# Performance work log

Hardware: AMD Instinct MI355X
Metric: run time of the kernel (lower is better)

Reference implementation:

```python
import jax, jax.numpy as jnp
import numpy as np

NR_EMB = 4096
D = 128
DECAY = 0.99
EPS = 1e-05
COMMITMENT_WEIGHT = 1.0


def setup_inputs() -> dict:
    key = jax.random.key(0)
    k1, k2 = jax.random.split(key)
    inpt = jax.random.normal(k1, (32, 2048, D), dtype=jnp.float32)
    emb_mtrx = jax.random.normal(k2, (D, NR_EMB), dtype=jnp.float32) * 0.05
    ema_cluster_size = jnp.zeros((NR_EMB,), dtype=jnp.float32)
    ema_dw = emb_mtrx  # build() initializes ema_dw to a copy of emb_mtrx
    return {"inpt": inpt, "emb_mtrx": emb_mtrx,
            "ema_cluster_size": ema_cluster_size, "ema_dw": ema_dw}


def reference(inpt, emb_mtrx, ema_cluster_size, ema_dw):
    # training=True forward: quantize + EMA codebook update
    K = emb_mtrx.shape[1]
    x = inpt.reshape(-1, inpt.shape[-1])  # [N, D]
    dist = (jnp.sum(x * x, axis=1, keepdims=True)
            - 2.0 * (x @ emb_mtrx)
            + jnp.sum(emb_mtrx * emb_mtrx, axis=0, keepdims=True))  # [N, K]
    idx = jnp.argmax(-dist, axis=1)                       # [N]
    idx_oh = jax.nn.one_hot(idx, K, dtype=x.dtype)        # [N, K]

    # EMA updates (moving_average_update: s = s*decay + v*(1-decay))
    new_cluster = ema_cluster_size * DECAY + jnp.sum(idx_oh, axis=0) * (1.0 - DECAY)
    new_dw = ema_dw * DECAY + (x.T @ idx_oh) * (1.0 - DECAY)  # [D, K]
    n = jnp.sum(new_cluster)
    new_emb = new_dw / (n * (new_cluster + 1e-05) / (n + K * 1e-05))[None, :]

    # lookup uses the just-updated codebook (assign happens before lookup in TF eager)
    idx_r = idx.reshape(inpt.shape[:-1])
    q = new_emb.T[idx_r]                                  # [B, T, D]

    l_commitment = jnp.mean((jax.lax.stop_gradient(q) - inpt) ** 2)
    loss = COMMITMENT_WEIGHT * l_commitment
    q = inpt + jax.lax.stop_gradient(q - inpt)            # straight-through

    avg_probs = jnp.mean(idx_oh, axis=0)
    perplexity = jnp.exp(-jnp.sum(avg_probs * jnp.log(avg_probs + 1e-10)))
    return q, loss, perplexity, new_emb, new_cluster, new_dw
```

## Files before the change

### kernel.cpp

```cpp
#include <hip/hip_runtime.h>
#include <cstdint>
#include <cstddef>

#define NR_EMB 4096
#define DD 128
#define NTOT 65536
#define MARGIN 3e-4f
#define RB 16

typedef __attribute__((ext_vector_type(8))) short short8;
typedef __attribute__((ext_vector_type(4))) float f32x4;

#define WS_CNT    0u
#define WS_SCAL   16384u
#define WS_AMBC   16448u
#define WS_COLN   16512u
#define WS_IDX    32896u
#define WS_EMBT   295040u
#define WS_LPART  2392192u
#define WS_ETH    2424960u
#define WS_ETL    3473536u
#define WS_AMBL   4522112u
#define WS_OFF    4784256u
#define WS_CUR    4800640u
#define WS_BKT    4817024u
#define WS_DWT    5079168u

#define OUT_Q      0u
#define OUT_LOSS   8388608u
#define OUT_PERP   8388609u
#define OUT_EMB    8388610u
#define OUT_CLUS   8912898u
#define OUT_DW     8916994u

__device__ __forceinline__ unsigned short f2bf(float f) {
    unsigned u = __float_as_uint(f);
    return (unsigned short)((u + 0x7FFFu + ((u >> 16) & 1u)) >> 16);
}
__device__ __forceinline__ float bf2f(unsigned short h) {
    return __uint_as_float(((unsigned)h) << 16);
}

__global__ __launch_bounds__(128) void k_prep_e(const float* __restrict__ E,
                                                unsigned short* __restrict__ EtHb,
                                                unsigned short* __restrict__ EtLb,
                                                float* __restrict__ coln,
                                                unsigned int* __restrict__ counts,
                                                int* __restrict__ ambC) {
    __shared__ float Es[128][33];
    const int tid = threadIdx.x;
    const int k0  = blockIdx.x * 32;
    if (tid < 32) counts[k0 + tid] = 0u;
    if (blockIdx.x == 0 && tid < 16) ambC[tid] = 0;
    #pragma unroll
    for (int i = 0; i < 32; ++i) {
        int e = i * 128 + tid;
        int d = e >> 5, kc = e & 31;
        Es[d][kc] = E[(size_t)d * NR_EMB + k0 + kc];
    }
    __syncthreads();
    const int kc = tid >> 2, q = tid & 3;
    const int k = k0 + kc;
    const int sw = (k & 7) << 3;
    float cs = 0.f;
    #pragma unroll
    for (int i = 0; i < 32; ++i) {
        float v = Es[q * 32 + i][kc];
        cs = fmaf(v, v, cs);
    }
    #pragma unroll
    for (int j = 0; j < 4; ++j) {
        short8 hv, lv;
        #pragma unroll
        for (int e = 0; e < 8; ++e) {
            int od = q * 32 + j * 8 + e;
            float v = Es[od ^ sw][kc];
            unsigned short h = f2bf(v);
            hv[e] = (short)h;
            lv[e] = (short)f2bf(v - bf2f(h));
        }
        *(short8*)&EtHb[(size_t)k * DD + q * 32 + j * 8] = hv;
        *(short8*)&EtLb[(size_t)k * DD + q * 32 + j * 8] = lv;
    }
    cs += __shfl_xor(cs, 1);
    cs += __shfl_xor(cs, 2);
    if (q == 0) coln[k] = cs;
}

__device__ __forceinline__ void mrg(float& b1, int& i1, float& b2,
                                    float ob1, int oi1, float ob2) {
    bool take = (ob1 < b1) || (ob1 == b1 && oi1 < i1);
    float loser = take ? b1 : ob1;
    b2 = fminf(fminf(b2, ob2), loser);
    if (take) { b1 = ob1; i1 = oi1; }
}

__global__ __launch_bounds__(256, 2) void k_dist(const float* __restrict__ x,
                                                 const unsigned short* __restrict__ EtHb,
                                                 const unsigned short* __restrict__ EtLb,
                                                 const float* __restrict__ coln,
                                                 int* __restrict__ idx_out,
                                                 unsigned int* __restrict__ counts,
                                                 int* __restrict__ ambCnt,
                                                 int* __restrict__ ambList) {
    __shared__ char lds[65536];

    const int tid  = threadIdx.x;
    const int lane = tid & 63;
    const int w    = tid >> 6;
    const int n0   = blockIdx.x * 128;
    const int rowbase = (w >> 1) * 32;
    const int shalf   = (w & 1) * 64;

    auto stage = [&](int kt, int b) {
        const char* gH = (const char*)EtHb + (size_t)kt * 16384;
        const char* gL = (const char*)EtLb + (size_t)kt * 16384;
        char* lH = lds + b * 32768;
        char* lL = lH + 16384;
        int off = tid * 16;
        #pragma unroll
        for (int j = 0; j < 4; ++j) {
            __builtin_amdgcn_global_load_lds(
                (const __attribute__((address_space(1))) unsigned int*)(gH + off + j * 4096),
                (__attribute__((address_space(3))) unsigned int*)(lH + off + j * 4096), 16, 0, 0);
            __builtin_amdgcn_global_load_lds(
                (const __attribute__((address_space(1))) unsigned int*)(gL + off + j * 4096),
                (__attribute__((address_space(3))) unsigned int*)(lL + off + j * 4096), 16, 0, 0);
        }
    };

    stage(0, 0);

    short8 ah[4][4], al[4][4];
    #pragma unroll
    for (int m = 0; m < 4; ++m) {
        int samp = n0 + shalf + m * 16 + (lane & 15);
        const float* xp = x + (size_t)samp * DD + ((lane >> 4) * 8);
        #pragma unroll
        for (int t = 0; t < 4; ++t) {
            float4 f0 = *(const float4*)(xp + t * 32);
            float4 f1 = *(const float4*)(xp + t * 32 + 4);
            float fv[8] = {f0.x, f0.y, f0.z, f0.w, f1.x, f1.y, f1.z, f1.w};
            short8 h, l;
            #pragma unroll
            for (int j = 0; j < 8; ++j) {
                unsigned short hh = f2bf(fv[j]);
                h[j] = (short)hh;
                l[j] = (short)f2bf(fv[j] - bf2f(hh));
            }
            ah[m][t] = h;
            al[m][t] = l;
        }
    }
    __syncthreads();

    float b1[4][4], b2[4][4];
    int   kb[4][4];
    #pragma unroll
    for (int m = 0; m < 4; ++m)
        #pragma unroll
        for (int r = 0; r < 4; ++r) { b1[m][r] = 3.4e38f; b2[m][r] = 3.4e38f; kb[m][r] = 0; }

    int buf = 0;
    for (int kt = 0; kt < 64; ++kt) {
        if (kt < 63) stage(kt + 1, buf ^ 1);
        const char* lH = lds + buf * 32768;
        const char* lL = lH + 16384;

        #pragma unroll
        for (int n = 0; n < 2; ++n) {
            int row = rowbase + n * 16 + (lane & 15);
            size_t rbo = (size_t)row << 8;
            unsigned swz = (unsigned)((row & 7) << 4);
            float cn = coln[kt * 64 + row];
            int enc = kt * 2 + n;

            f32x4 acc[4];
            #pragma unroll
            for (int m = 0; m < 4; ++m) acc[m] = (f32x4){0.f, 0.f, 0.f, 0.f};

            __builtin_amdgcn_s_setprio(1);
            #pragma unroll
            for (int t = 0; t < 4; ++t) {
                unsigned coff = ((unsigned)(t * 64 + ((lane >> 4) << 4))) ^ swz;
                short8 bh = *(const short8*)(lH + rbo + coff);
                short8 bl = *(const short8*)(lL + rbo + coff);
                #pragma unroll
                for (int m = 0; m < 4; ++m)
                    acc[m] = __builtin_amdgcn_mfma_f32_16x16x32_bf16(ah[m][t], bh, acc[m], 0, 0, 0);
                #pragma unroll
                for (int m = 0; m < 4; ++m)
                    acc[m] = __builtin_amdgcn_mfma_f32_16x16x32_bf16(al[m][t], bh, acc[m], 0, 0, 0);
                #pragma unroll
                for (int m = 0; m < 4; ++m)
                    acc[m] = __builtin_amdgcn_mfma_f32_16x16x32_bf16(ah[m][t], bl, acc[m], 0, 0, 0);
            }
            __builtin_amdgcn_s_setprio(0);

            #pragma unroll
            for (int m = 0; m < 4; ++m) {
                #pragma unroll
                for (int r = 0; r < 4; ++r) {
                    float d = fmaf(-2.f, acc[m][r], cn);
                    bool lt = d < b1[m][r];
                    b2[m][r] = __builtin_amdgcn_fmed3f(d, b1[m][r], b2[m][r]);
                    b1[m][r] = fminf(b1[m][r], d);
                    kb[m][r] = lt ? enc : kb[m][r];
                }
            }
        }
        __syncthreads();
        buf ^= 1;
    }

    float* sb1 = (float*)lds;
    int*   si1 = (int*)(lds + 1024);
    float* sb2 = (float*)(lds + 2048);

    #pragma unroll
    for (int m = 0; m < 4; ++m) {
        #pragma unroll
        for (int r = 0; r < 4; ++r) {
            float B1 = b1[m][r];
            int   I1 = (kb[m][r] >> 1) * 64 + rowbase + (kb[m][r] & 1) * 16 + (lane & 15);
            float B2 = b2[m][r];
            #pragma unroll
            for (int msk = 1; msk < 16; msk <<= 1) {
                float ob1 = __shfl_xor(B1, msk);
                int   oi1 = __shfl_xor(I1, msk);
                float ob2 = __shfl_xor(B2, msk);
                mrg(B1, I1, B2, ob1, oi1, ob2);
            }
            if ((lane & 15) == 0) {
                int sl = shalf + m * 16 + ((lane >> 4) << 2) + r;
                int ch = w >> 1;
                sb1[ch * 128 + sl] = B1;
                si1[ch * 128 + sl] = I1;
                sb2[ch * 128 + sl] = B2;
            }
        }
    }
    __syncthreads();
    if (tid < 128) {
        float B1 = sb1[tid]; int I1 = si1[tid]; float B2 = sb2[tid];
        mrg(B1, I1, B2, sb1[128 + tid], si1[128 + tid], sb2[128 + tid]);
        idx_out[n0 + tid] = I1;
        atomicAdd(&counts[I1], 1u);
        if (B2 - B1 < MARGIN) {
            int p = atomicAdd(ambCnt, 1);
            ambList[p] = n0 + tid;
        }
    }
}

__global__ __launch_bounds__(256) void k_rescore(const float* __restrict__ x,
                                                 const float* __restrict__ E,
                                                 const float* __restrict__ coln,
                                                 const int* __restrict__ ambCnt,
                                                 const int* __restrict__ ambList,
                                                 float* __restrict__ pval,
                                                 int* __restrict__ pidx) {
    __shared__ float xs[RB][DD];
    __shared__ float xn[RB];
    __shared__ float rb1[RB][256];
    __shared__ int   ri1[RB][256];

    const int tid = threadIdx.x;
    const int cnt = *ambCnt;
    const int nbatch = (cnt + RB - 1) / RB;
    const int nwork = nbatch * 8;

    for (int wk = blockIdx.x; wk < nwork; wk += gridDim.x) {
        const int b  = wk >> 3;
        const int ch = wk & 7;
        const int e0 = b * RB;
        const int nb = min(RB, cnt - e0);
        __syncthreads();
        #pragma unroll
        for (int p = 0; p < 2; ++p) {
            int slot = p * 256 + tid;
            int e = slot >> 5, c = slot & 31;
            if (e < nb) {
                int s = ambList[e0 + e];
                *(float4*)&xs[e][c * 4] = *(const float4*)&x[(size_t)s * DD + c * 4];
            } else {
                float4 z; z.x = z.y = z.z = z.w = 0.f;
                *(float4*)&xs[e][c * 4] = z;
            }
        }
        __syncthreads();
        if (tid < RB) {
            float a = 0.f;
            for (int d = 0; d < DD; ++d) a = fmaf(xs[tid][d], xs[tid][d], a);
            xn[tid] = a;
        }
        __syncthreads();

        const int ka  = ch * 512 + tid;
        const int kb2 = ka + 256;
        const float* Ea = E + ka;
        const float* Eb = E + kb2;
        float acca[RB], accb[RB];
        #pragma unroll
        for (int e = 0; e < RB; ++e) { acca[e] = 0.f; accb[e] = 0.f; }

        float4 cA, cB, nA, nB;
        {
            cA.x = Ea[0];                  cA.y = Ea[(size_t)1 * NR_EMB];
            cA.z = Ea[(size_t)2 * NR_EMB]; cA.w = Ea[(size_t)3 * NR_EMB];
            cB.x = Eb[0];                  cB.y = Eb[(size_t)1 * NR_EMB];
            cB.z = Eb[(size_t)2 * NR_EMB]; cB.w = Eb[(size_t)3 * NR_EMB];
            const size_t d1 = (size_t)4 * NR_EMB;
            nA.x = Ea[d1];                nA.y = Ea[d1 + NR_EMB];
            nA.z = Ea[d1 + 2 * NR_EMB];   nA.w = Ea[d1 + 3 * NR_EMB];
            nB.x = Eb[d1];                nB.y = Eb[d1 + NR_EMB];
            nB.z = Eb[d1 + 2 * NR_EMB];   nB.w = Eb[d1 + 3 * NR_EMB];
        }

        for (int d4 = 0; d4 < 30; ++d4) {
            float4 fA, fB;
            const size_t dn = (size_t)(d4 * 4 + 8) * NR_EMB;
            fA.x = Ea[dn];                fA.y = Ea[dn + NR_EMB];
            fA.z = Ea[dn + 2 * NR_EMB];   fA.w = Ea[dn + 3 * NR_EMB];
            fB.x = Eb[dn];                fB.y = Eb[dn + NR_EMB];
            fB.z = Eb[dn + 2 * NR_EMB];   fB.w = Eb[dn + 3 * NR_EMB];
            #pragma unroll
            for (int e = 0; e < RB; ++e) {
                float4 xv = *(const float4*)&xs[e][d4 * 4];
                acca[e] = fmaf(xv.x, cA.x, acca[e]);
                acca[e] = fmaf(xv.y, cA.y, acca[e]);
                acca[e] = fmaf(xv.z, cA.z, acca[e]);
                acca[e] = fmaf(xv.w, cA.w, acca[e]);
                accb[e] = fmaf(xv.x, cB.x, accb[e]);
                accb[e] = fmaf(xv.y, cB.y, accb[e]);
                accb[e] = fmaf(xv.z, cB.z, accb[e]);
                accb[e] = fmaf(xv.w, cB.w, accb[e]);
            }
            cA = nA; cB = nB; nA = fA; nB = fB;
        }
        #pragma unroll
        for (int e = 0; e < RB; ++e) {
            float4 xv = *(const float4*)&xs[e][120];
            acca[e] = fmaf(xv.x, cA.x, acca[e]);
            acca[e] = fmaf(xv.y, cA.y, acca[e]);
            acca[e] = fmaf(xv.z, cA.z, acca[e]);
            acca[e] = fmaf(xv.w, cA.w, acca[e]);
            accb[e] = fmaf(xv.x, cB.x, accb[e]);
            accb[e] = fmaf(xv.y, cB.y, accb[e]);
            accb[e] = fmaf(xv.z, cB.z, accb[e]);
            accb[e] = fmaf(xv.w, cB.w, accb[e]);
        }
        #pragma unroll
        for (int e = 0; e < RB; ++e) {
            float4 xv = *(const float4*)&xs[e][124];
            acca[e] = fmaf(xv.x, nA.x, acca[e]);
            acca[e] = fmaf(xv.y, nA.y, acca[e]);
            acca[e] = fmaf(xv.z, nA.z, acca[e]);
            acca[e] = fmaf(xv.w, nA.w, acca[e]);
            accb[e] = fmaf(xv.x, nB.x, accb[e]);
            accb[e] = fmaf(xv.y, nB.y, accb[e]);
            accb[e] = fmaf(xv.z, nB.z, accb[e]);
            accb[e] = fmaf(xv.w, nB.w, accb[e]);
        }

        const float cna = coln[ka];
        const float cnb = coln[kb2];
        float b1[RB]; int i1[RB];
        #pragma unroll
        for (int e = 0; e < RB; ++e) {
            float da = (xn[e] - 2.0f * acca[e]) + cna;
            float db = (xn[e] - 2.0f * accb[e]) + cnb;
            bool ltb = db < da;
            b1[e] = ltb ? db : da;
            i1[e] = ltb ? kb2 : ka;
        }

        #pragma unroll
        for (int e = 0; e < RB; ++e) { rb1[e][tid] = b1[e]; ri1[e][tid] = i1[e]; }
        __syncthreads();
        {
            int g = tid >> 4, l = tid & 15;
            float B = rb1[g][l]; int I = ri1[g][l];
            #pragma unroll
            for (int j = 1; j < 16; ++j) {
                float ob = rb1[g][l + 16 * j]; int oi = ri1[g][l + 16 * j];
                if (ob < B || (ob == B && oi < I)) { B = ob; I = oi; }
            }
            #pragma unroll
            for (int m = 1; m < 16; m <<= 1) {
                float ob = __shfl_xor(B, m, 16);
                int   oi = __shfl_xor(I, m, 16);
                if (ob < B || (ob == B && oi < I)) { B = ob; I = oi; }
            }
            if (l == 0 && g < nb) {
                pval[wk * RB + g] = B;
                pidx[wk * RB + g] = I;
            }
        }
    }
}

__global__ __launch_bounds__(256) void k_rfinal(const int* __restrict__ ambCnt,
                                                const int* __restrict__ ambList,
                                                const float* __restrict__ pval,
                                                const int* __restrict__ pidx,
                                                int* __restrict__ idx_out,
                                                unsigned int* __restrict__ counts) {
    const int cnt = *ambCnt;
    for (int i = blockIdx.x * 256 + threadIdx.x; i < cnt; i += gridDim.x * 256) {
        int b = i >> 4, g = i & 15;
        float B = pval[(b * 8) * RB + g];
        int   I = pidx[(b * 8) * RB + g];
        #pragma unroll
        for (int ch = 1; ch < 8; ++ch) {
            float ob = pval[(b * 8 + ch) * RB + g];
            int   oi = pidx[(b * 8 + ch) * RB + g];
            if (ob < B || (ob == B && oi < I)) { B = ob; I = oi; }
        }
        int s = ambList[i];
        int old = idx_out[s];
        if (I != old) {
            atomicSub(&counts[old], 1u);
            atomicAdd(&counts[I], 1u);
            idx_out[s] = I;
        }
    }
}

__global__ __launch_bounds__(256) void k_statsprefix(const float* __restrict__ emaC,
                                                     const unsigned int* __restrict__ counts,
                                                     float* __restrict__ outC,
                                                     float* __restrict__ scal,
                                                     float* __restrict__ outPerp,
                                                     int* __restrict__ off,
                                                     int* __restrict__ cursor) {
    __shared__ float rs[256], rp[256];
    __shared__ int rc[256];
    const int tid = threadIdx.x;
    float sc = 0.f, sp = 0.f;
    int csum = 0;
    int lc[16];
    #pragma unroll
    for (int j = 0; j < 16; ++j) {
        int k = tid * 16 + j;
        int c = (int)counts[k];
        lc[j] = csum; csum += c;
        float nc = emaC[k] * 0.99f + (float)c * 0.01f;
        outC[k] = nc;
        sc += nc;
        float p = (float)c * (1.0f / 65536.0f);
        sp += p * logf(p + 1e-10f);
    }
    rs[tid] = sc; rp[tid] = sp; rc[tid] = csum;
    __syncthreads();
    for (int o = 1; o < 256; o <<= 1) {
        int v = (tid >= o) ? rc[tid - o] : 0;
        __syncthreads();
        rc[tid] += v;
        __syncthreads();
    }
    const int base = rc[tid] - csum;
    #pragma unroll
    for (int j = 0; j < 16; ++j) {
        int k = tid * 16 + j;
        int o = base + lc[j];
        off[k] = o;
        cursor[k] = o;
    }
    for (int o = 128; o > 0; o >>= 1) {
        if (tid < o) { rs[tid] += rs[tid + o]; rp[tid] += rp[tid + o]; }
        __syncthreads();
    }
    if (tid == 0) {
        scal[0] = rs[0];
        outPerp[0] = expf(-rp[0]);
    }
}

__global__ __launch_bounds__(256) void k_fill(const int* __restrict__ idx,
                                              int* __restrict__ cursor,
                                              int* __restrict__ bucket) {
    for (int i = blockIdx.x * 256 + threadIdx.x; i < NTOT; i += gridDim.x * 256) {
        int k = idx[i];
        int p = atomicAdd(&cursor[k], 1);
        bucket[p] = i;
    }
}

__global__ __launch_bounds__(128) void k_dw(const float* __restrict__ x,
                                            const int* __restrict__ off,
                                            const unsigned int* __restrict__ counts,
                                            const int* __restrict__ bucket,
                                            float* __restrict__ dwT) {
    const int k = blockIdx.x;
    const int d = threadIdx.x;
    const int o = off[k];
    const int c = (int)counts[k];
    float acc = 0.f;
    if (c > 0) {
        int s0 = bucket[o];
        int s1 = (c > 1) ? bucket[o + 1] : 0;
        int p = 0;
        for (; p < c - 2; ++p) {
            int s2 = bucket[o + p + 2];
            acc += x[(size_t)s0 * DD + d];
            s0 = s1; s1 = s2;
        }
        acc += x[(size_t)s0 * DD + d];
        if (c > 1) acc += x[(size_t)s1 * DD + d];
    }
    dwT[(size_t)k * DD + d] = acc;
}

__global__ __launch_bounds__(256) void k_emb(const float* __restrict__ emaDw,
                                             const float* __restrict__ emaC,
                                             const unsigned int* __restrict__ counts,
                                             const float* __restrict__ dwT,
                                             const float* __restrict__ scal,
                                             float* __restrict__ outDw,
                                             float* __restrict__ outEmb,
                                             float* __restrict__ embT) {
    int g = blockIdx.x * 256 + threadIdx.x;
    int d = g >> 12;
    int k = g & 4095;
    float dw  = emaDw[g] * 0.99f + dwT[k * DD + d] * 0.01f;
    float cnt = (float)counts[k];
    float nc  = emaC[k] * 0.99f + cnt * 0.01f;
    float n   = scal[0];
    float denom = n * (nc + 1e-5f) / (n + 0.04096f);
    float e = dw / denom;
    outDw[g]  = dw;
    outEmb[g] = e;
    embT[k * DD + d] = e;
}

__global__ __launch_bounds__(256) void k_gather(const float* __restrict__ x,
                                                const float* __restrict__ embT,
                                                const int* __restrict__ idx,
                                                float* __restrict__ q,
                                                float* __restrict__ lpart) {
    __shared__ float wred[4];
    int g = blockIdx.x * 256 + threadIdx.x;
    int n = g >> 4;
    int c = g & 15;
    int k = idx[n];
    const float* ep = &embT[(size_t)k * DD + c * 8];
    const float* xp = &x[(size_t)n * DD + c * 8];
    float4 e0 = *(const float4*)(ep);
    float4 e1 = *(const float4*)(ep + 4);
    float4 x0 = *(const float4*)(xp);
    float4 x1 = *(const float4*)(xp + 4);
    float s = 0.f;
    float4 q0, q1;
    {
        float dx = e0.x - x0.x, dy = e0.y - x0.y, dz = e0.z - x0.z, dw = e0.w - x0.w;
        q0.x = x0.x + dx; q0.y = x0.y + dy; q0.z = x0.z + dz; q0.w = x0.w + dw;
        s += dx * dx + dy * dy + dz * dz + dw * dw;
    }
    {
        float dx = e1.x - x1.x, dy = e1.y - x1.y, dz = e1.z - x1.z, dw = e1.w - x1.w;
        q1.x = x1.x + dx; q1.y = x1.y + dy; q1.z = x1.z + dz; q1.w = x1.w + dw;
        s += dx * dx + dy * dy + dz * dz + dw * dw;
    }
    float* qp = &q[(size_t)n * DD + c * 8];
    *(float4*)(qp)     = q0;
    *(float4*)(qp + 4) = q1;
    #pragma unroll
    for (int off = 32; off > 0; off >>= 1) s += __shfl_down(s, off);
    if ((threadIdx.x & 63) == 0) wred[threadIdx.x >> 6] = s;
    __syncthreads();
    if (threadIdx.x == 0)
        lpart[blockIdx.x] = wred[0] + wred[1] + wred[2] + wred[3];
}

__global__ __launch_bounds__(256) void k_final(const float* __restrict__ lpart,
                                               float* __restrict__ outLoss) {
    __shared__ float r[256];
    float s = 0.f;
    for (int i = threadIdx.x; i < 4096; i += 256) s += lpart[i];
    r[threadIdx.x] = s;
    __syncthreads();
    for (int off = 128; off > 0; off >>= 1) {
        if (threadIdx.x < off) r[threadIdx.x] += r[threadIdx.x + off];
        __syncthreads();
    }
    if (threadIdx.x == 0) outLoss[0] = r[0] * (1.0f / 8388608.0f);
}

extern "C" void kernel_launch(void* const* d_in, const int* in_sizes, int n_in,
                              void* d_out, int out_size, void* d_ws, size_t ws_size,
                              hipStream_t stream) {
    const float* x     = (const float*)d_in[0];
    const float* E     = (const float*)d_in[1];
    const float* emaC  = (const float*)d_in[2];
    const float* emaDw = (const float*)d_in[3];
    float* out = (float*)d_out;
    char*  ws  = (char*)d_ws;

    unsigned int*   cnts  = (unsigned int*)(ws + WS_CNT);
    float*          scal  = (float*)(ws + WS_SCAL);
    int*            ambC  = (int*)(ws + WS_AMBC);
    float*          coln  = (float*)(ws + WS_COLN);
    int*            idx   = (int*)(ws + WS_IDX);
    float*          embT  = (float*)(ws + WS_EMBT);
    float*          lpart = (float*)(ws + WS_LPART);
    unsigned short* EtHb  = (unsigned short*)(ws + WS_ETH);
    unsigned short* EtLb  = (unsigned short*)(ws + WS_ETL);
    int*            ambL  = (int*)(ws + WS_AMBL);
    int*            off   = (int*)(ws + WS_OFF);
    int*            cur   = (int*)(ws + WS_CUR);
    int*            bkt   = (int*)(ws + WS_BKT);
    float*          dwT   = (float*)(ws + WS_DWT);

    float* pval = dwT;
    int*   pidx = (int*)embT;

    k_prep_e<<<128, 128, 0, stream>>>(E, EtHb, EtLb, coln, cnts, ambC);
    k_dist<<<NTOT / 128, 256, 0, stream>>>(x, EtHb, EtLb, coln, idx, cnts, ambC, ambL);
    k_rescore<<<2048, 256, 0, stream>>>(x, E, coln, ambC, ambL, pval, pidx);
    k_rfinal<<<64, 256, 0, stream>>>(ambC, ambL, pval, pidx, idx, cnts);
    k_statsprefix<<<1, 256, 0, stream>>>(emaC, cnts, out + OUT_CLUS, scal, out + OUT_PERP,
                                         off, cur);
    k_fill<<<256, 256, 0, stream>>>(idx, cur, bkt);
    k_dw<<<NR_EMB, 128, 0, stream>>>(x, off, cnts, bkt, dwT);
    k_emb<<<(DD * NR_EMB) / 256, 256, 0, stream>>>(emaDw, emaC, cnts, dwT, scal,
                                                   out + OUT_DW, out + OUT_EMB, embT);
    k_gather<<<(NTOT * DD / 8) / 256, 256, 0, stream>>>(x, embT, idx, out + OUT_Q, lpart);
    k_final<<<1, 256, 0, stream>>>(lpart, out + OUT_LOSS);
}
```

Before: 265.3 us.

## Split distance kernel across two codebook halves and merge partial argmins

The distance/argmin kernel now splits the codebook into two halves, launching 1024 blocks that each scan 2048 codes over 32-row tiles with half the LDS. Partial best/second-best values and indices go to workspace, and a new merge kernel combines them and takes over the index write, histogram and ambiguous-list work. This raises block count and occupancy (smaller LDS) to fill the GPU better. The cost is x being reloaded and converted twice, an extra kernel launch, and extra global traffic for the partial results.

```diff
diff --git a/kernel.cpp b/kernel.cpp
--- a/kernel.cpp
+++ b/kernel.cpp
@@ -99,27 +99,29 @@
                                                  const unsigned short* __restrict__ EtHb,
                                                  const unsigned short* __restrict__ EtLb,
                                                  const float* __restrict__ coln,
-                                                 int* __restrict__ idx_out,
-                                                 unsigned int* __restrict__ counts,
-                                                 int* __restrict__ ambCnt,
-                                                 int* __restrict__ ambList) {
-    __shared__ char lds[65536];
+                                                 float* __restrict__ pb1,
+                                                 int* __restrict__ pi1,
+                                                 float* __restrict__ pb2) {
+    __shared__ char lds[32768];
 
     const int tid  = threadIdx.x;
     const int lane = tid & 63;
     const int w    = tid >> 6;
-    const int n0   = blockIdx.x * 128;
-    const int rowbase = (w >> 1) * 32;
+    const int g    = blockIdx.x & 511;
+    const int kh   = blockIdx.x >> 9;
+    const int n0   = g * 128;
+    const int kbase = kh * 2048;
+    const int rowbase = (w >> 1) * 16;
     const int shalf   = (w & 1) * 64;
 
     auto stage = [&](int kt, int b) {
-        const char* gH = (const char*)EtHb + (size_t)kt * 16384;
-        const char* gL = (const char*)EtLb + (size_t)kt * 16384;
-        char* lH = lds + b * 32768;
-        char* lL = lH + 16384;
+        const char* gH = (const char*)EtHb + (size_t)kbase * 256 + (size_t)kt * 8192;
+        const char* gL = (const char*)EtLb + (size_t)kbase * 256 + (size_t)kt * 8192;
+        char* lH = lds + b * 16384;
+        char* lL = lH + 8192;
         int off = tid * 16;
         #pragma unroll
-        for (int j = 0; j < 4; ++j) {
+        for (int j = 0; j < 2; ++j) {
             __builtin_amdgcn_global_load_lds(
                 (const __attribute__((address_space(1))) unsigned int*)(gH + off + j * 4096),
                 (__attribute__((address_space(3))) unsigned int*)(lH + off + j * 4096), 16, 0, 0);
@@ -161,52 +163,48 @@
         #pragma unroll
         for (int r = 0; r < 4; ++r) { b1[m][r] = 3.4e38f; b2[m][r] = 3.4e38f; kb[m][r] = 0; }
 
+    const int row = rowbase + (lane & 15);
+    const size_t rbo = (size_t)row << 8;
+    const unsigned swz = (unsigned)((row & 7) << 4);
+
     int buf = 0;
     for (int kt = 0; kt < 64; ++kt) {
         if (kt < 63) stage(kt + 1, buf ^ 1);
-        const char* lH = lds + buf * 32768;
-        const char* lL = lH + 16384;
-
-        #pragma unroll
-        for (int n = 0; n < 2; ++n) {
-            int row = rowbase + n * 16 + (lane & 15);
-            size_t rbo = (size_t)row << 8;
-            unsigned swz = (unsigned)((row & 7) << 4);
-            float cn = coln[kt * 64 + row];
-            int enc = kt * 2 + n;
-
-            f32x4 acc[4];
-            #pragma unroll
-            for (int m = 0; m < 4; ++m) acc[m] = (f32x4){0.f, 0.f, 0.f, 0.f};
-
-            __builtin_amdgcn_s_setprio(1);
-            #pragma unroll
-            for (int t = 0; t < 4; ++t) {
-                unsigned coff = ((unsigned)(t * 64 + ((lane >> 4) << 4))) ^ swz;
-                short8 bh = *(const short8*)(lH + rbo + coff);
-                short8 bl = *(const short8*)(lL + rbo + coff);
-                #pragma unroll
-                for (int m = 0; m < 4; ++m)
-                    acc[m] = __builtin_amdgcn_mfma_f32_16x16x32_bf16(ah[m][t], bh, acc[m], 0, 0, 0);
-                #pragma unroll
-                for (int m = 0; m < 4; ++m)
-                    acc[m] = __builtin_amdgcn_mfma_f32_16x16x32_bf16(al[m][t], bh, acc[m], 0, 0, 0);
-                #pragma unroll
-                for (int m = 0; m < 4; ++m)
-                    acc[m] = __builtin_amdgcn_mfma_f32_16x16x32_bf16(ah[m][t], bl, acc[m], 0, 0, 0);
-            }
-            __builtin_amdgcn_s_setprio(0);
-
-            #pragma unroll
-            for (int m = 0; m < 4; ++m) {
-                #pragma unroll
-                for (int r = 0; r < 4; ++r) {
-                    float d = fmaf(-2.f, acc[m][r], cn);
-                    bool lt = d < b1[m][r];
-                    b2[m][r] = __builtin_amdgcn_fmed3f(d, b1[m][r], b2[m][r]);
-                    b1[m][r] = fminf(b1[m][r], d);
-                    kb[m][r] = lt ? enc : kb[m][r];
-                }
+        const char* lH = lds + buf * 16384;
+        const char* lL = lH + 8192;
+        float cn = coln[kbase + kt * 32 + row];
+
+        f32x4 acc[4];
+        #pragma unroll
+        for (int m = 0; m < 4; ++m) acc[m] = (f32x4){0.f, 0.f, 0.f, 0.f};
+
+        __builtin_amdgcn_s_setprio(1);
+        #pragma unroll
+        for (int t = 0; t < 4; ++t) {
+            unsigned coff = ((unsigned)(t * 64 + ((lane >> 4) << 4))) ^ swz;
+            short8 bh = *(const short8*)(lH + rbo + coff);
+            short8 bl = *(const short8*)(lL + rbo + coff);
+            #pragma unroll
+            for (int m = 0; m < 4; ++m)
+                acc[m] = __builtin_amdgcn_mfma_f32_16x16x32_bf16(ah[m][t], bh, acc[m], 0, 0, 0);
+            #pragma unroll
+            for (int m = 0; m < 4; ++m)
+                acc[m] = __builtin_amdgcn_mfma_f32_16x16x32_bf16(al[m][t], bh, acc[m], 0, 0, 0);
+            #pragma unroll
+            for (int m = 0; m < 4; ++m)
+                acc[m] = __builtin_amdgcn_mfma_f32_16x16x32_bf16(ah[m][t], bl, acc[m], 0, 0, 0);
+        }
+        __builtin_amdgcn_s_setprio(0);
+
+        #pragma unroll
+        for (int m = 0; m < 4; ++m) {
+            #pragma unroll
+            for (int r = 0; r < 4; ++r) {
+                float d = fmaf(-2.f, acc[m][r], cn);
+                bool lt = d < b1[m][r];
+                b2[m][r] = __builtin_amdgcn_fmed3f(d, b1[m][r], b2[m][r]);
+                b1[m][r] = fminf(b1[m][r], d);
+                kb[m][r] = lt ? kt : kb[m][r];
             }
         }
         __syncthreads();
@@ -222,7 +220,7 @@
         #pragma unroll
         for (int r = 0; r < 4; ++r) {
             float B1 = b1[m][r];
-            int   I1 = (kb[m][r] >> 1) * 64 + rowbase + (kb[m][r] & 1) * 16 + (lane & 15);
+            int   I1 = kbase + kb[m][r] * 32 + rowbase + (lane & 15);
             float B2 = b2[m][r];
             #pragma unroll
             for (int msk = 1; msk < 16; msk <<= 1) {
@@ -244,11 +242,28 @@
     if (tid < 128) {
         float B1 = sb1[tid]; int I1 = si1[tid]; float B2 = sb2[tid];
         mrg(B1, I1, B2, sb1[128 + tid], si1[128 + tid], sb2[128 + tid]);
-        idx_out[n0 + tid] = I1;
+        int s = n0 + tid;
+        pb1[kh * NTOT + s] = B1;
+        pi1[kh * NTOT + s] = I1;
+        pb2[kh * NTOT + s] = B2;
+    }
+}
+
+__global__ __launch_bounds__(256) void k_merge(const float* __restrict__ pb1,
+                                               const int* __restrict__ pi1,
+                                               const float* __restrict__ pb2,
+                                               int* __restrict__ idx_out,
+                                               unsigned int* __restrict__ counts,
+                                               int* __restrict__ ambCnt,
+                                               int* __restrict__ ambList) {
+    for (int i = blockIdx.x * 256 + threadIdx.x; i < NTOT; i += gridDim.x * 256) {
+        float B1 = pb1[i];           int I1 = pi1[i];           float B2 = pb2[i];
+        mrg(B1, I1, B2, pb1[NTOT + i], pi1[NTOT + i], pb2[NTOT + i]);
+        idx_out[i] = I1;
         atomicAdd(&counts[I1], 1u);
         if (B2 - B1 < MARGIN) {
             int p = atomicAdd(ambCnt, 1);
-            ambList[p] = n0 + tid;
+            ambList[p] = i;
         }
     }
 }
@@ -612,11 +627,15 @@
     int*            bkt   = (int*)(ws + WS_BKT);
     float*          dwT   = (float*)(ws + WS_DWT);
 
+    float* pb1 = dwT;
+    float* pb2 = dwT + 2 * NTOT;
+    int*   pi1 = (int*)embT;
     float* pval = dwT;
     int*   pidx = (int*)embT;
 
     k_prep_e<<<128, 128, 0, stream>>>(E, EtHb, EtLb, coln, cnts, ambC);
-    k_dist<<<NTOT / 128, 256, 0, stream>>>(x, EtHb, EtLb, coln, idx, cnts, ambC, ambL);
+    k_dist<<<1024, 256, 0, stream>>>(x, EtHb, EtLb, coln, pb1, pi1, pb2);
+    k_merge<<<256, 256, 0, stream>>>(pb1, pi1, pb2, idx, cnts, ambC, ambL);
     k_rescore<<<2048, 256, 0, stream>>>(x, E, coln, ambC, ambL, pval, pidx);
     k_rfinal<<<64, 256, 0, stream>>>(ambC, ambL, pval, pidx, idx, cnts);
     k_statsprefix<<<1, 256, 0, stream>>>(emaC, cnts, out + OUT_CLUS, scal, out + OUT_PERP,
```

After: 285.9 us. 7.8% more time.
